# Optimization experiments

Hardware: AMD Instinct MI355X
Metric: run time of the kernel (lower is better)

Reference implementation:

```python
import jax, jax.numpy as jnp
from jax import lax
import numpy as np

B, S, D = 8, 128, 512      # batch, seq (tweets per profile), hidden_size
N = 64                     # attention_neurons
H = 128                    # lstm_size


def _lstm(x, Wih, Whh, bih, bhh):
    """Standard torch-gate-order LSTM (i,f,g,o). x: [B,S,Din] -> [B,S,H]."""
    b = x.shape[0]
    h_dim = Whh.shape[1]
    xt = jnp.swapaxes(x, 0, 1)                      # [S,B,Din]
    gx = xt @ Wih.T + (bih + bhh)                   # precompute input gates [S,B,4H]

    def step(carry, g_in):
        h, c = carry
        g = g_in + h @ Whh.T
        i, f, gg, o = jnp.split(g, 4, axis=-1)
        i, f, o = jax.nn.sigmoid(i), jax.nn.sigmoid(f), jax.nn.sigmoid(o)
        gg = jnp.tanh(gg)
        c = f * c + i * gg
        h = o * jnp.tanh(c)
        return (h, c), h

    h0 = jnp.zeros((b, h_dim), x.dtype)
    _, hs = lax.scan(step, (h0, h0), gx)
    return jnp.swapaxes(hs, 0, 1)                   # [B,S,H]


def setup_inputs() -> dict:
    key = jax.random.key(0)
    ks = jax.random.split(key, 24)
    g = lambda k, shp, s: jax.random.normal(k, shp, dtype=jnp.float32) * s
    inp = {
        "A": g(ks[0], (B, S, D), 1.0),
        # AttentionLSTM params
        "Wx_W": g(ks[1], (N, D), 1.0 / np.sqrt(D)), "Wx_b": g(ks[2], (N,), 0.01),
        "Wxh_W": g(ks[3], (N, D), 1.0 / np.sqrt(D)), "Wxh_b": g(ks[4], (N,), 0.01),
        "Att_W": g(ks[5], (1, N), 1.0 / np.sqrt(N)), "Att_b": g(ks[6], (1,), 0.01),
        # BiLSTM (forward + reverse directions)
        "Wih_f": g(ks[7], (4 * H, D), 1.0 / np.sqrt(H)), "Whh_f": g(ks[8], (4 * H, H), 1.0 / np.sqrt(H)),
        "bih_f": g(ks[9], (4 * H,), 0.01), "bhh_f": g(ks[10], (4 * H,), 0.01),
        "Wih_r": g(ks[11], (4 * H, D), 1.0 / np.sqrt(H)), "Whh_r": g(ks[12], (4 * H, H), 1.0 / np.sqrt(H)),
        "bih_r": g(ks[13], (4 * H,), 0.01), "bhh_r": g(ks[14], (4 * H,), 0.01),
        # second (uni) LSTM: input 2H -> H
        "Wih2": g(ks[15], (4 * H, 2 * H), 1.0 / np.sqrt(H)), "Whh2": g(ks[16], (4 * H, H), 1.0 / np.sqrt(H)),
        "bih2": g(ks[17], (4 * H,), 0.01), "bhh2": g(ks[18], (4 * H,), 0.01),
        # dense (H->32) and classifier (32->2)
        "dense_W": g(ks[19], (32, H), 1.0 / np.sqrt(H)), "dense_b": g(ks[20], (32,), 0.01),
        "clf_W": g(ks[21], (2, 32), 1.0 / np.sqrt(32)), "clf_b": g(ks[22], (2,), 0.01),
    }
    return inp


def reference(A, Wx_W, Wx_b, Wxh_W, Wxh_b, Att_W, Att_b,
              Wih_f, Whh_f, bih_f, bhh_f, Wih_r, Whh_r, bih_r, bhh_r,
              Wih2, Whh2, bih2, bhh2, dense_W, dense_b, clf_W, clf_b):
    # --- AttentionLSTM ---
    # torch builds Wthat[b,i,j,:]=A[b,j,:] ([B,S,S,D]); Wxhat = Linear(Wthat) is
    # independent of i, so project once and broadcast (same math, no SxSxD blowup).
    Wx = A @ Wx_W.T + Wx_b                            # [B,S,N] (query-side)
    Px = A @ Wxh_W.T + Wxh_b                          # [B,S,N] (key-side)
    t = jnp.tanh(Px[:, None, :, :] + Wx[:, :, None, :])  # [B,S,S,N]
    scores = jax.nn.sigmoid(jnp.einsum('bijn,n->bij', t, Att_W[0]) + Att_b[0])  # [B,S,S]
    X = jnp.einsum('bij,bjd->bid', scores, A)         # sum_j A[b,j]*score -> [B,S,D]

    # --- BiLSTM ---
    hf = _lstm(X, Wih_f, Whh_f, bih_f, bhh_f)                         # [B,S,H]
    hr = _lstm(X[:, ::-1], Wih_r, Whh_r, bih_r, bhh_r)[:, ::-1]       # [B,S,H]
    Xb = jnp.concatenate([hf, hr], axis=-1)                           # [B,S,2H]

    # --- second LSTM, last step ---
    h2 = _lstm(Xb, Wih2, Whh2, bih2, bhh2)[:, -1]                     # [B,H]

    # --- MLP head ---
    z = h2 @ dense_W.T + dense_b                                      # [B,32]
    return z @ clf_W.T + clf_b                                        # [B,2]
```

## Files before the change

kernel.cpp:

```cpp
#include <hip/hip_runtime.h>
#include <hip/hip_bf16.h>

#define B_ 8
#define S_ 128
#define D_ 512
#define N_ 64
#define H_ 128

#define OFF_WX      0
#define OFF_PX      65536
#define OFF_X       131072
#define OFF_GXF     655360
#define OFF_GXR     1179648
#define OFF_HF      1703936
#define OFF_HR      1835008
#define OFF_GX2     1966080
#define OFF_WIHTQ_F 2490368
#define OFF_WIHTQ_R 2752512
#define OFF_WIHT2Q  3014656
#define OFF_WHHT_F  3145728
#define OFF_WHHT_R  3211264
#define OFF_WHHT2   3276800
#define OFF_BIASF   3342336
#define OFF_BIASR   3342848
#define OFF_BIAS2   3343360

__device__ __forceinline__ float rlane(float v, int l) {
    return __int_as_float(__builtin_amdgcn_readlane(__float_as_int(v), l));
}
__device__ __forceinline__ float sigf(float x) {
    return 1.0f / (1.0f + expf(-x));
}

__global__ __launch_bounds__(256) void k_prep(
    const float* __restrict__ Wih_f, const float* __restrict__ Wih_r,
    const float* __restrict__ Wih2,
    const float* __restrict__ Whh_f, const float* __restrict__ Whh_r,
    const float* __restrict__ Whh2,
    const float* __restrict__ bih_f, const float* __restrict__ bhh_f,
    const float* __restrict__ bih_r, const float* __restrict__ bhh_r,
    const float* __restrict__ bih2, const float* __restrict__ bhh2,
    float* __restrict__ wihTq_f, float* __restrict__ wihTq_r,
    float* __restrict__ wihT2q,
    float* __restrict__ whhT_f, float* __restrict__ whhT_r,
    float* __restrict__ whhT2,
    float* __restrict__ biasf, float* __restrict__ biasr, float* __restrict__ bias2)
{
    int idx = blockIdx.x * blockDim.x + threadIdx.x;
    int stride = gridDim.x * blockDim.x;
    for (int o = idx; o < 262144; o += stride) {
        int q = o >> 11, rem = o & 2047, j = rem >> 2, e = rem & 3;
        int k = 4 * q + e;
        wihTq_f[o] = Wih_f[j * 512 + k];
        wihTq_r[o] = Wih_r[j * 512 + k];
    }
    for (int o = idx; o < 131072; o += stride) {
        int q = o >> 11, rem = o & 2047, j = rem >> 2, e = rem & 3;
        int k = 4 * q + e;
        wihT2q[o] = Wih2[j * 256 + k];
    }
    for (int o = idx; o < 65536; o += stride) {
        int k = o >> 9, j = o & 511;
        whhT_f[o] = Whh_f[j * 128 + k];
        whhT_r[o] = Whh_r[j * 128 + k];
        whhT2[o]  = Whh2[j * 128 + k];
    }
    if (idx < 512) {
        biasf[idx] = bih_f[idx] + bhh_f[idx];
        biasr[idx] = bih_r[idx] + bhh_r[idx];
        bias2[idx] = bih2[idx] + bhh2[idx];
    }
}

__global__ __launch_bounds__(64) void k_qk(
    const float* __restrict__ A,
    const float* __restrict__ WxW, const float* __restrict__ Wxb,
    const float* __restrict__ WxhW, const float* __restrict__ Wxhb,
    float* __restrict__ WX, float* __restrict__ PX)
{
    int bs = blockIdx.x;
    int n = threadIdx.x;
    const float* arow = A + bs * 512;
    const float* wr = WxW + n * 512;
    const float* pr = WxhW + n * 512;
    float aw = 0.f, ap = 0.f;
    #pragma unroll 8
    for (int k = 0; k < 512; k += 4) {
        float4 a = *(const float4*)(arow + k);
        float4 w = *(const float4*)(wr + k);
        float4 p = *(const float4*)(pr + k);
        aw += a.x * w.x + a.y * w.y + a.z * w.z + a.w * w.w;
        ap += a.x * p.x + a.y * p.y + a.z * p.z + a.w * p.w;
    }
    WX[bs * 64 + n] = aw + Wxb[n];
    PX[bs * 64 + n] = ap + Wxhb[n];
}

__global__ __launch_bounds__(256) void k_attn(
    const float* __restrict__ A,
    const float* __restrict__ WX, const float* __restrict__ PX,
    const float* __restrict__ AttW, const float* __restrict__ Attb,
    float* __restrict__ X)
{
    int b = blockIdx.x >> 5;
    int i0 = (blockIdx.x & 31) * 4;
    int tid = threadIdx.x;
    __shared__ float px[128][65];
    __shared__ float wx[4][64];
    __shared__ float aw[64];
    __shared__ float sc[128][4];

    const float* pxg = PX + b * 8192;
    for (int q = tid; q < 2048; q += 256) {
        int j = q >> 4, nq = (q & 15) * 4;
        float4 v = *(const float4*)(pxg + j * 64 + nq);
        px[j][nq] = v.x; px[j][nq + 1] = v.y; px[j][nq + 2] = v.z; px[j][nq + 3] = v.w;
    }
    if (tid < 64) {
        aw[tid] = AttW[tid];
        #pragma unroll
        for (int ii = 0; ii < 4; ii++)
            wx[ii][tid] = WX[b * 8192 + (i0 + ii) * 64 + tid];
    }
    __syncthreads();
    float attb = Attb[0];
    for (int p = tid; p < 512; p += 256) {
        int ii = p >> 7, j = p & 127;
        float acc = 0.f;
        #pragma unroll 4
        for (int n = 0; n < 64; n++) {
            acc += tanhf(px[j][n] + wx[ii][n]) * aw[n];
        }
        sc[j][ii] = sigf(acc + attb);
    }
    __syncthreads();
    int half = tid >> 7;
    int dq = (tid & 127) * 4;
    int ii0 = half * 2;
    float4 acc0 = {0, 0, 0, 0}, acc1 = {0, 0, 0, 0};
    const float* Ab = A + b * 65536;
    for (int j = 0; j < 128; j++) {
        float4 av = *(const float4*)(Ab + j * 512 + dq);
        float s0 = sc[j][ii0], s1 = sc[j][ii0 + 1];
        acc0.x += av.x * s0; acc0.y += av.y * s0; acc0.z += av.z * s0; acc0.w += av.w * s0;
        acc1.x += av.x * s1; acc1.y += av.y * s1; acc1.z += av.z * s1; acc1.w += av.w * s1;
    }
    float* Xp = X + b * 65536;
    *(float4*)(Xp + (i0 + ii0) * 512 + dq) = acc0;
    *(float4*)(Xp + (i0 + ii0 + 1) * 512 + dq) = acc1;
}

__global__ __launch_bounds__(512) void k_gx(
    const float* __restrict__ X,
    const float* __restrict__ wihTq_f, const float* __restrict__ wihTq_r,
    const float* __restrict__ biasf, const float* __restrict__ biasr,
    float* __restrict__ GXF, float* __restrict__ GXR)
{
    int r0 = blockIdx.x * 8;
    int j = threadIdx.x;
    float bf = biasf[j], br = biasr[j];
    float af[8], ar[8];
    #pragma unroll
    for (int s = 0; s < 8; s++) { af[s] = bf; ar[s] = br; }
    for (int q = 0; q < 128; q++) {
        float4 wf = *(const float4*)(wihTq_f + q * 2048 + j * 4);
        float4 wr = *(const float4*)(wihTq_r + q * 2048 + j * 4);
        #pragma unroll
        for (int s = 0; s < 8; s++) {
            float4 xv = *(const float4*)(X + (r0 + s) * 512 + 4 * q);
            af[s] += xv.x * wf.x + xv.y * wf.y + xv.z * wf.z + xv.w * wf.w;
            ar[s] += xv.x * wr.x + xv.y * wr.y + xv.z * wr.z + xv.w * wr.w;
        }
    }
    #pragma unroll
    for (int s = 0; s < 8; s++) {
        int r = r0 + s, b = r >> 7, ss = r & 127;
        GXF[r * 512 + j] = af[s];
        GXR[(b * 128 + (127 - ss)) * 512 + j] = ar[s];
    }
}

__global__ __launch_bounds__(512, 2) void k_lstm_bi(
    const float* __restrict__ GXF, const float* __restrict__ GXR,
    const float* __restrict__ whhT_f, const float* __restrict__ whhT_r,
    float* __restrict__ HF, float* __restrict__ HR)
{
    int dir = blockIdx.x & 1, b = blockIdx.x >> 1;
    int j = threadIdx.x;
    int lane = j & 63;
    const float* whhT = dir ? whhT_r : whhT_f;
    const float* gx = (dir ? GXR : GXF) + b * 65536;
    float* hout = (dir ? HR : HF) + b * 16384;

    float w[128];
    #pragma unroll
    for (int k = 0; k < 128; k++) w[k] = whhT[k * 512 + j];

    __shared__ float gbuf[512];
    __shared__ float hbuf[128];
    float c = 0.f;
    float h_lo = 0.f, h_hi = 0.f;
    float g = gx[j];
    for (int t = 0; t < 128; t++) {
        float a = g;
        if (t < 127) g = gx[(t + 1) * 512 + j];
        #pragma unroll
        for (int k = 0; k < 64; k++) a += rlane(h_lo, k) * w[k];
        #pragma unroll
        for (int k = 0; k < 64; k++) a += rlane(h_hi, k) * w[64 + k];
        gbuf[j] = a;
        __syncthreads();
        if (j < 128) {
            float ig = sigf(a);
            float fg = sigf(gbuf[128 + j]);
            float gg = tanhf(gbuf[256 + j]);
            float og = sigf(gbuf[384 + j]);
            c = fg * c + ig * gg;
            float hn = og * tanhf(c);
            hbuf[j] = hn;
            int tout = dir ? (127 - t) : t;
            hout[tout * 128 + j] = hn;
        }
        __syncthreads();
        h_lo = hbuf[lane];
        h_hi = hbuf[64 + lane];
    }
}

__global__ __launch_bounds__(512) void k_gx2(
    const float* __restrict__ HF, const float* __restrict__ HR,
    const float* __restrict__ wihT2q, const float* __restrict__ bias2,
    float* __restrict__ GX2)
{
    int r0 = blockIdx.x * 8;
    int j = threadIdx.x;
    float bb = bias2[j];
    float a[8];
    #pragma unroll
    for (int s = 0; s < 8; s++) a[s] = bb;
    for (int q = 0; q < 32; q++) {
        float4 w = *(const float4*)(wihT2q + q * 2048 + j * 4);
        #pragma unroll
        for (int s = 0; s < 8; s++) {
            int r = r0 + s;
            float4 xv = *(const float4*)(HF + r * 128 + 4 * q);
            a[s] += xv.x * w.x + xv.y * w.y + xv.z * w.z + xv.w * w.w;
        }
    }
    for (int q = 32; q < 64; q++) {
        float4 w = *(const float4*)(wihT2q + q * 2048 + j * 4);
        #pragma unroll
        for (int s = 0; s < 8; s++) {
            int r = r0 + s;
            float4 xv = *(const float4*)(HR + r * 128 + 4 * q - 128);
            a[s] += xv.x * w.x + xv.y * w.y + xv.z * w.z + xv.w * w.w;
        }
    }
    #pragma unroll
    for (int s = 0; s < 8; s++) GX2[(r0 + s) * 512 + j] = a[s];
}

__global__ __launch_bounds__(512, 2) void k_lstm2(
    const float* __restrict__ GX2, const float* __restrict__ whhT2,
    const float* __restrict__ denseW, const float* __restrict__ denseb,
    const float* __restrict__ clfW, const float* __restrict__ clfb,
    float* __restrict__ out)
{
    int b = blockIdx.x;
    int j = threadIdx.x;
    int lane = j & 63;
    const float* gx = GX2 + b * 65536;

    float w[128];
    #pragma unroll
    for (int k = 0; k < 128; k++) w[k] = whhT2[k * 512 + j];

    __shared__ float gbuf[512];
    __shared__ float hbuf[128];
    float c = 0.f;
    float h_lo = 0.f, h_hi = 0.f;
    float g = gx[j];
    for (int t = 0; t < 128; t++) {
        float a = g;
        if (t < 127) g = gx[(t + 1) * 512 + j];
        #pragma unroll
        for (int k = 0; k < 64; k++) a += rlane(h_lo, k) * w[k];
        #pragma unroll
        for (int k = 0; k < 64; k++) a += rlane(h_hi, k) * w[64 + k];
        gbuf[j] = a;
        __syncthreads();
        if (j < 128) {
            float ig = sigf(a);
            float fg = sigf(gbuf[128 + j]);
            float gg = tanhf(gbuf[256 + j]);
            float og = sigf(gbuf[384 + j]);
            c = fg * c + ig * gg;
            float hn = og * tanhf(c);
            hbuf[j] = hn;
        }
        __syncthreads();
        h_lo = hbuf[lane];
        h_hi = hbuf[64 + lane];
    }
    __shared__ float z[32];
    if (j < 32) {
        float acc = denseb[j];
        const float* dw = denseW + j * 128;
        for (int k = 0; k < 128; k++) acc += hbuf[k] * dw[k];
        z[j] = acc;
    }
    __syncthreads();
    if (j < 2) {
        float acc = clfb[j];
        const float* cw = clfW + j * 32;
        #pragma unroll
        for (int m = 0; m < 32; m++) acc += z[m] * cw[m];
        out[b * 2 + j] = acc;
    }
}

extern "C" void kernel_launch(void* const* d_in, const int* in_sizes, int n_in,
                              void* d_out, int out_size, void* d_ws, size_t ws_size,
                              hipStream_t stream) {
    const float* A     = (const float*)d_in[0];
    const float* Wx_W  = (const float*)d_in[1];
    const float* Wx_b  = (const float*)d_in[2];
    const float* Wxh_W = (const float*)d_in[3];
    const float* Wxh_b = (const float*)d_in[4];
    const float* Att_W = (const float*)d_in[5];
    const float* Att_b = (const float*)d_in[6];
    const float* Wih_f = (const float*)d_in[7];
    const float* Whh_f = (const float*)d_in[8];
    const float* bih_f = (const float*)d_in[9];
    const float* bhh_f = (const float*)d_in[10];
    const float* Wih_r = (const float*)d_in[11];
    const float* Whh_r = (const float*)d_in[12];
    const float* bih_r = (const float*)d_in[13];
    const float* bhh_r = (const float*)d_in[14];
    const float* Wih2  = (const float*)d_in[15];
    const float* Whh2  = (const float*)d_in[16];
    const float* bih2  = (const float*)d_in[17];
    const float* bhh2  = (const float*)d_in[18];
    const float* denseW = (const float*)d_in[19];
    const float* denseb = (const float*)d_in[20];
    const float* clfW   = (const float*)d_in[21];
    const float* clfb   = (const float*)d_in[22];

    float* ws = (float*)d_ws;
    float* WXb    = ws + OFF_WX;
    float* PXb    = ws + OFF_PX;
    float* Xb     = ws + OFF_X;
    float* GXF    = ws + OFF_GXF;
    float* GXR    = ws + OFF_GXR;
    float* HF     = ws + OFF_HF;
    float* HR     = ws + OFF_HR;
    float* GX2    = ws + OFF_GX2;
    float* wihTqf = ws + OFF_WIHTQ_F;
    float* wihTqr = ws + OFF_WIHTQ_R;
    float* wihT2q = ws + OFF_WIHT2Q;
    float* whhTf  = ws + OFF_WHHT_F;
    float* whhTr  = ws + OFF_WHHT_R;
    float* whhT2  = ws + OFF_WHHT2;
    float* biasf  = ws + OFF_BIASF;
    float* biasr  = ws + OFF_BIASR;
    float* bias2  = ws + OFF_BIAS2;

    k_prep<<<512, 256, 0, stream>>>(Wih_f, Wih_r, Wih2, Whh_f, Whh_r, Whh2,
                                    bih_f, bhh_f, bih_r, bhh_r, bih2, bhh2,
                                    wihTqf, wihTqr, wihT2q, whhTf, whhTr, whhT2,
                                    biasf, biasr, bias2);
    k_qk<<<B_ * S_, 64, 0, stream>>>(A, Wx_W, Wx_b, Wxh_W, Wxh_b, WXb, PXb);
    k_attn<<<B_ * (S_ / 4), 256, 0, stream>>>(A, WXb, PXb, Att_W, Att_b, Xb);
    k_gx<<<128, 512, 0, stream>>>(Xb, wihTqf, wihTqr, biasf, biasr, GXF, GXR);
    k_lstm_bi<<<16, 512, 0, stream>>>(GXF, GXR, whhTf, whhTr, HF, HR);
    k_gx2<<<128, 512, 0, stream>>>(HF, HR, wihT2q, bias2, GX2);
    k_lstm2<<<B_, 512, 0, stream>>>(GX2, whhT2, denseW, denseb, clfW, clfb,
                                    (float*)d_out);
}
```

Before: 513.9 us.

## Run LSTM recurrences on MFMA with split-bf16 weights, batching all sequences per block

The recurrent h@Whh step in both LSTM kernels moves from per-thread fp32 FMAs with readlane broadcasts to bf16 MFMA 16x16x32. Weights and hidden state are split into hi/lo bf16 parts to approximate fp32 precision, using three MFMA passes. All 8 batch rows are now processed in one block per direction, so the grids shrink from 16 and 8 blocks to 2 and 1. This cuts per-step FMA and readlane latency on the serial critical path, at the cost of less parallelism across CUs and a small precision loss from the split-bf16 scheme.

```diff
diff --git a/kernel.cpp b/kernel.cpp
--- a/kernel.cpp
+++ b/kernel.cpp
@@ -10,26 +10,31 @@
 #define OFF_WX      0
 #define OFF_PX      65536
 #define OFF_X       131072
+#define OFF_GX2     131072
 #define OFF_GXF     655360
 #define OFF_GXR     1179648
 #define OFF_HF      1703936
 #define OFF_HR      1835008
-#define OFF_GX2     1966080
+#define OFF_BPKF    1966080
+#define OFF_BPKR    2064384
+#define OFF_BPK2    2162688
 #define OFF_WIHTQ_F 2490368
 #define OFF_WIHTQ_R 2752512
 #define OFF_WIHT2Q  3014656
-#define OFF_WHHT_F  3145728
-#define OFF_WHHT_R  3211264
-#define OFF_WHHT2   3276800
 #define OFF_BIASF   3342336
 #define OFF_BIASR   3342848
 #define OFF_BIAS2   3343360
 
-__device__ __forceinline__ float rlane(float v, int l) {
-    return __int_as_float(__builtin_amdgcn_readlane(__float_as_int(v), l));
-}
-__device__ __forceinline__ float sigf(float x) {
-    return 1.0f / (1.0f + expf(-x));
+typedef short bf16x8 __attribute__((ext_vector_type(8)));
+typedef float f32x4 __attribute__((ext_vector_type(4)));
+
+__device__ __forceinline__ float sigf(float x) { return 1.0f / (1.0f + expf(-x)); }
+__device__ __forceinline__ unsigned short f2bf(float x) {
+    unsigned u = __float_as_uint(x);
+    return (unsigned short)((u + 0x7FFFu + ((u >> 16) & 1u)) >> 16);
+}
+__device__ __forceinline__ float bf2f(unsigned short h) {
+    return __uint_as_float(((unsigned)h) << 16);
 }
 
 __global__ __launch_bounds__(256) void k_prep(
@@ -42,8 +47,8 @@
     const float* __restrict__ bih2, const float* __restrict__ bhh2,
     float* __restrict__ wihTq_f, float* __restrict__ wihTq_r,
     float* __restrict__ wihT2q,
-    float* __restrict__ whhT_f, float* __restrict__ whhT_r,
-    float* __restrict__ whhT2,
+    unsigned short* __restrict__ BpkF, unsigned short* __restrict__ BpkR,
+    unsigned short* __restrict__ Bpk2,
     float* __restrict__ biasf, float* __restrict__ biasr, float* __restrict__ bias2)
 {
     int idx = blockIdx.x * blockDim.x + threadIdx.x;
@@ -59,11 +64,20 @@
         int k = 4 * q + e;
         wihT2q[o] = Wih2[j * 256 + k];
     }
-    for (int o = idx; o < 65536; o += stride) {
-        int k = o >> 9, j = o & 511;
-        whhT_f[o] = Whh_f[j * 128 + k];
-        whhT_r[o] = Whh_r[j * 128 + k];
-        whhT2[o]  = Whh2[j * 128 + k];
+    for (int o = idx; o < 196608; o += stride) {
+        int e = o & 7, hi = (o >> 3) & 3, n = (o >> 5) & 511, kf = o >> 14;
+        int kcat = kf * 32 + hi * 8 + e;
+        int k = kcat & 127;
+        bool mid = (kcat >= 128) && (kcat < 256);
+        float wf = Whh_f[n * 128 + k];
+        unsigned short h1 = f2bf(wf);
+        BpkF[o] = mid ? f2bf(wf - bf2f(h1)) : h1;
+        float wr = Whh_r[n * 128 + k];
+        unsigned short h2 = f2bf(wr);
+        BpkR[o] = mid ? f2bf(wr - bf2f(h2)) : h2;
+        float w2 = Whh2[n * 128 + k];
+        unsigned short h3 = f2bf(w2);
+        Bpk2[o] = mid ? f2bf(w2 - bf2f(h3)) : h3;
     }
     if (idx < 512) {
         biasf[idx] = bih_f[idx] + bhh_f[idx];
@@ -180,51 +194,125 @@
     }
 }
 
-__global__ __launch_bounds__(512, 2) void k_lstm_bi(
-    const float* __restrict__ GXF, const float* __restrict__ GXR,
-    const float* __restrict__ whhT_f, const float* __restrict__ whhT_r,
-    float* __restrict__ HF, float* __restrict__ HR)
-{
-    int dir = blockIdx.x & 1, b = blockIdx.x >> 1;
-    int j = threadIdx.x;
-    int lane = j & 63;
-    const float* whhT = dir ? whhT_r : whhT_f;
-    const float* gx = (dir ? GXR : GXF) + b * 65536;
-    float* hout = (dir ? HR : HF) + b * 16384;
-
-    float w[128];
+#define PINB(kf) asm volatile("" : "+a"(bfr[kf][0]), "+a"(bfr[kf][1]), "+a"(bfr[kf][2]), "+a"(bfr[kf][3]));
+
+template<int DO_HOUT, int DO_FIN>
+__device__ __forceinline__ void lstm_core(
+    const float* __restrict__ gx,
+    const unsigned short* __restrict__ Bpk,
+    float* __restrict__ hout,
+    int rev,
+    float (*gatebuf)[128][8],
+    unsigned short (*ahi)[136], unsigned short (*alo)[136],
+    float (*hfin)[128])
+{
+    int tid = threadIdx.x;
+    int w = tid >> 6;
+    int l = tid & 63;
+    int lo4 = l & 15, hi4 = l >> 4;
+
+    bf16x8 bfr[12][4];
     #pragma unroll
-    for (int k = 0; k < 128; k++) w[k] = whhT[k * 512 + j];
-
-    __shared__ float gbuf[512];
-    __shared__ float hbuf[128];
-    float c = 0.f;
-    float h_lo = 0.f, h_hi = 0.f;
-    float g = gx[j];
+    for (int kf = 0; kf < 12; kf++)
+        #pragma unroll
+        for (int nt = 0; nt < 4; nt++) {
+            int n = w * 64 + nt * 16 + lo4;
+            bfr[kf][nt] = *(const bf16x8*)(Bpk + (((kf * 512 + n) * 4 + hi4) << 3));
+        }
+    PINB(0) PINB(1) PINB(2) PINB(3) PINB(4) PINB(5)
+    PINB(6) PINB(7) PINB(8) PINB(9) PINB(10) PINB(11)
+
+    for (int i = tid; i < 8 * 136; i += 512) {
+        ((unsigned short*)ahi)[i] = 0;
+        ((unsigned short*)alo)[i] = 0;
+    }
+    int hh0 = tid >> 3, bb = tid & 7;
+    float c0 = 0.f, c1 = 0.f;
+    __syncthreads();
+
     for (int t = 0; t < 128; t++) {
-        float a = g;
-        if (t < 127) g = gx[(t + 1) * 512 + j];
-        #pragma unroll
-        for (int k = 0; k < 64; k++) a += rlane(h_lo, k) * w[k];
-        #pragma unroll
-        for (int k = 0; k < 64; k++) a += rlane(h_hi, k) * w[64 + k];
-        gbuf[j] = a;
+        float gxp[8];
+        const float* gxt = gx + (bb * 128 + t) * 512;
+        #pragma unroll
+        for (int gti = 0; gti < 4; gti++) {
+            gxp[gti]     = gxt[gti * 128 + hh0];
+            gxp[4 + gti] = gxt[gti * 128 + hh0 + 64];
+        }
+
+        f32x4 acc[4];
+        #pragma unroll
+        for (int nt = 0; nt < 4; nt++) acc[nt] = (f32x4){0.f, 0.f, 0.f, 0.f};
+        #pragma unroll
+        for (int g = 0; g < 3; g++) {
+            bf16x8 af[4];
+            #pragma unroll
+            for (int kk = 0; kk < 4; kk++) {
+                const unsigned short* src = (g < 2) ? &ahi[l & 7][kk * 32 + hi4 * 8]
+                                                    : &alo[l & 7][kk * 32 + hi4 * 8];
+                af[kk] = *(const bf16x8*)src;
+            }
+            #pragma unroll
+            for (int kk = 0; kk < 4; kk++)
+                #pragma unroll
+                for (int nt = 0; nt < 4; nt++)
+                    acc[nt] = __builtin_amdgcn_mfma_f32_16x16x32_bf16(
+                        af[kk], bfr[g * 4 + kk][nt], acc[nt], 0, 0, 0);
+        }
+
+        if (hi4 < 2) {
+            int gtype = w >> 1;
+            int hb = (w & 1) * 64;
+            #pragma unroll
+            for (int nt = 0; nt < 4; nt++)
+                *(f32x4*)&gatebuf[gtype][hb + nt * 16 + lo4][hi4 * 4] = acc[nt];
+        }
         __syncthreads();
-        if (j < 128) {
-            float ig = sigf(a);
-            float fg = sigf(gbuf[128 + j]);
-            float gg = tanhf(gbuf[256 + j]);
-            float og = sigf(gbuf[384 + j]);
-            c = fg * c + ig * gg;
-            float hn = og * tanhf(c);
-            hbuf[j] = hn;
-            int tout = dir ? (127 - t) : t;
-            hout[tout * 128 + j] = hn;
+
+        {
+            float iv = gatebuf[0][hh0][bb] + gxp[0];
+            float fv = gatebuf[1][hh0][bb] + gxp[1];
+            float gv = gatebuf[2][hh0][bb] + gxp[2];
+            float ov = gatebuf[3][hh0][bb] + gxp[3];
+            c0 = sigf(fv) * c0 + sigf(iv) * tanhf(gv);
+            float hn = sigf(ov) * tanhf(c0);
+            unsigned short hhi = f2bf(hn);
+            unsigned short hlo = f2bf(hn - bf2f(hhi));
+            ahi[bb][hh0] = hhi;
+            alo[bb][hh0] = hlo;
+            if (DO_HOUT) hout[(bb * 128 + (rev ? 127 - t : t)) * 128 + hh0] = hn;
+            if (DO_FIN) hfin[bb][hh0] = hn;
+        }
+        {
+            int hh = hh0 + 64;
+            float iv = gatebuf[0][hh][bb] + gxp[4];
+            float fv = gatebuf[1][hh][bb] + gxp[5];
+            float gv = gatebuf[2][hh][bb] + gxp[6];
+            float ov = gatebuf[3][hh][bb] + gxp[7];
+            c1 = sigf(fv) * c1 + sigf(iv) * tanhf(gv);
+            float hn = sigf(ov) * tanhf(c1);
+            unsigned short hhi = f2bf(hn);
+            unsigned short hlo = f2bf(hn - bf2f(hhi));
+            ahi[bb][hh] = hhi;
+            alo[bb][hh] = hlo;
+            if (DO_HOUT) hout[(bb * 128 + (rev ? 127 - t : t)) * 128 + hh] = hn;
+            if (DO_FIN) hfin[bb][hh] = hn;
         }
         __syncthreads();
-        h_lo = hbuf[lane];
-        h_hi = hbuf[64 + lane];
-    }
+    }
+}
+
+__global__ __attribute__((amdgpu_waves_per_eu(2, 2))) __launch_bounds__(512)
+void k_lstm_bi(const float* __restrict__ GXF, const float* __restrict__ GXR,
+               const unsigned short* __restrict__ BpkF,
+               const unsigned short* __restrict__ BpkR,
+               float* __restrict__ HF, float* __restrict__ HR)
+{
+    __shared__ __align__(16) float gatebuf[4][128][8];
+    __shared__ __align__(16) unsigned short ahi[8][136];
+    __shared__ __align__(16) unsigned short alo[8][136];
+    int dir = blockIdx.x;
+    lstm_core<1, 0>(dir ? GXR : GXF, dir ? BpkR : BpkF, dir ? HR : HF, dir,
+                    gatebuf, ahi, alo, nullptr);
 }
 
 __global__ __launch_bounds__(512) void k_gx2(
@@ -260,62 +348,35 @@
     for (int s = 0; s < 8; s++) GX2[(r0 + s) * 512 + j] = a[s];
 }
 
-__global__ __launch_bounds__(512, 2) void k_lstm2(
-    const float* __restrict__ GX2, const float* __restrict__ whhT2,
-    const float* __restrict__ denseW, const float* __restrict__ denseb,
-    const float* __restrict__ clfW, const float* __restrict__ clfb,
-    float* __restrict__ out)
-{
-    int b = blockIdx.x;
-    int j = threadIdx.x;
-    int lane = j & 63;
-    const float* gx = GX2 + b * 65536;
-
-    float w[128];
-    #pragma unroll
-    for (int k = 0; k < 128; k++) w[k] = whhT2[k * 512 + j];
-
-    __shared__ float gbuf[512];
-    __shared__ float hbuf[128];
-    float c = 0.f;
-    float h_lo = 0.f, h_hi = 0.f;
-    float g = gx[j];
-    for (int t = 0; t < 128; t++) {
-        float a = g;
-        if (t < 127) g = gx[(t + 1) * 512 + j];
-        #pragma unroll
-        for (int k = 0; k < 64; k++) a += rlane(h_lo, k) * w[k];
-        #pragma unroll
-        for (int k = 0; k < 64; k++) a += rlane(h_hi, k) * w[64 + k];
-        gbuf[j] = a;
-        __syncthreads();
-        if (j < 128) {
-            float ig = sigf(a);
-            float fg = sigf(gbuf[128 + j]);
-            float gg = tanhf(gbuf[256 + j]);
-            float og = sigf(gbuf[384 + j]);
-            c = fg * c + ig * gg;
-            float hn = og * tanhf(c);
-            hbuf[j] = hn;
-        }
-        __syncthreads();
-        h_lo = hbuf[lane];
-        h_hi = hbuf[64 + lane];
-    }
-    __shared__ float z[32];
-    if (j < 32) {
-        float acc = denseb[j];
-        const float* dw = denseW + j * 128;
-        for (int k = 0; k < 128; k++) acc += hbuf[k] * dw[k];
-        z[j] = acc;
-    }
+__global__ __attribute__((amdgpu_waves_per_eu(2, 2))) __launch_bounds__(512)
+void k_lstm2(const float* __restrict__ GX2, const unsigned short* __restrict__ Bpk2,
+             const float* __restrict__ denseW, const float* __restrict__ denseb,
+             const float* __restrict__ clfW, const float* __restrict__ clfb,
+             float* __restrict__ out)
+{
+    __shared__ __align__(16) float gatebuf[4][128][8];
+    __shared__ __align__(16) unsigned short ahi[8][136];
+    __shared__ __align__(16) unsigned short alo[8][136];
+    __shared__ float hfin[8][128];
+    __shared__ float zbuf[8][32];
+    lstm_core<0, 1>(GX2, Bpk2, nullptr, 0, gatebuf, ahi, alo, hfin);
     __syncthreads();
-    if (j < 2) {
-        float acc = clfb[j];
-        const float* cw = clfW + j * 32;
-        #pragma unroll
-        for (int m = 0; m < 32; m++) acc += z[m] * cw[m];
-        out[b * 2 + j] = acc;
+    int tid = threadIdx.x;
+    if (tid < 256) {
+        int b = tid >> 5, zj = tid & 31;
+        float acc = denseb[zj];
+        const float* dw = denseW + zj * 128;
+        for (int k = 0; k < 128; k++) acc += hfin[b][k] * dw[k];
+        zbuf[b][zj] = acc;
+    }
+    __syncthreads();
+    if (tid < 16) {
+        int b = tid >> 1, oj = tid & 1;
+        float acc = clfb[oj];
+        const float* cw = clfW + oj * 32;
+        #pragma unroll
+        for (int m = 0; m < 32; m++) acc += zbuf[b][m] * cw[m];
+        out[b * 2 + oj] = acc;
     }
 }
 
@@ -355,25 +416,26 @@
     float* HF     = ws + OFF_HF;
     float* HR     = ws + OFF_HR;
     float* GX2    = ws + OFF_GX2;
+    unsigned short* BpkF = (unsigned short*)(ws + OFF_BPKF);
+    unsigned short* BpkR = (unsigned short*)(ws + OFF_BPKR);
+    unsigned short* Bpk2 = (unsigned short*)(ws + OFF_BPK2);
     float* wihTqf = ws + OFF_WIHTQ_F;
     float* wihTqr = ws + OFF_WIHTQ_R;
     float* wihT2q = ws + OFF_WIHT2Q;
-    float* whhTf  = ws + OFF_WHHT_F;
-    float* whhTr  = ws + OFF_WHHT_R;
-    float* whhT2  = ws + OFF_WHHT2;
     float* biasf  = ws + OFF_BIASF;
     float* biasr  = ws + OFF_BIASR;
     float* bias2  = ws + OFF_BIAS2;
 
     k_prep<<<512, 256, 0, stream>>>(Wih_f, Wih_r, Wih2, Whh_f, Whh_r, Whh2,
                                     bih_f, bhh_f, bih_r, bhh_r, bih2, bhh2,
-                                    wihTqf, wihTqr, wihT2q, whhTf, whhTr, whhT2,
+                                    wihTqf, wihTqr, wihT2q,
+                                    BpkF, BpkR, Bpk2,
                                     biasf, biasr, bias2);
     k_qk<<<B_ * S_, 64, 0, stream>>>(A, Wx_W, Wx_b, Wxh_W, Wxh_b, WXb, PXb);
     k_attn<<<B_ * (S_ / 4), 256, 0, stream>>>(A, WXb, PXb, Att_W, Att_b, Xb);
     k_gx<<<128, 512, 0, stream>>>(Xb, wihTqf, wihTqr, biasf, biasr, GXF, GXR);
-    k_lstm_bi<<<16, 512, 0, stream>>>(GXF, GXR, whhTf, whhTr, HF, HR);
+    k_lstm_bi<<<2, 512, 0, stream>>>(GXF, GXR, BpkF, BpkR, HF, HR);
     k_gx2<<<128, 512, 0, stream>>>(HF, HR, wihT2q, bias2, GX2);
-    k_lstm2<<<B_, 512, 0, stream>>>(GX2, whhT2, denseW, denseb, clfW, clfb,
-                                    (float*)d_out);
-}
+    k_lstm2<<<1, 512, 0, stream>>>(GX2, Bpk2, denseW, denseb, clfW, clfb,
+                                   (float*)d_out);
+}
```

Result: slower. 759.2 us (+47.7%).
